# Kernel tuning notes

Measured on AMD Instinct MI355X. Metric: run time of the kernel, lower is better.

Reference implementation:

```python
import jax, jax.numpy as jnp
import numpy as np

B, N = 128, 1024            # batch, sample_count
MIN_S, MAX_S, STEP = 4.0, 104.0, 1.0  # scale range -> S = 101 scales
OUT_H, OUT_W = 200, 200     # output_size


def morlet_kernels():
    # scales = tf.range(min_scale, max_scale+1, step)
    scales = jnp.arange(MIN_S, MAX_S + 1.0, STEP, dtype=jnp.float32)  # (S,)
    t = jnp.arange(N, dtype=jnp.float32) - (N - 1.0) / 2.0            # centered time
    times = t[None, :] / scales[:, None]                               # (S, N)
    return jnp.exp(-0.5 * times ** 2) * jnp.cos(5.0 * times)          # morlet


def setup_inputs() -> dict:
    key = jax.random.key(0)
    x = jax.random.normal(key, (B, N), dtype=jnp.float32)
    kernels = morlet_kernels()  # (S, N), non-trainable param built in build()
    return {"x": x, "kernels": kernels}


def reference(x, kernels):
    # x: (B, N) signals; kernels: (S, N) scaled wavelets.
    # Original per-sample op: conv1d(kernels[S,N,1], filter=reverse(x)[N,1,1], SAME)
    # -> correlation of each wavelet row with the reversed signal (= convolution with x).
    n = x.shape[1]
    pad_l = (n - 1) // 2           # TF 'SAME' padding, stride 1, filter length n
    pad_r = (n - 1) - pad_l
    x_rev = x[:, ::-1]
    # One grouped conv: lhs=(S,1,N) NCW, rhs=(B,1,N) OIW -> out (S,B,N)
    res = jax.lax.conv_general_dilated(
        kernels[:, None, :], x_rev[:, None, :],
        window_strides=(1,), padding=[(pad_l, pad_r)],
        dimension_numbers=("NCW", "OIW", "NCW"))
    res = jnp.transpose(res, (1, 0, 2))  # (B, S, N)
    # global (per-sample) min-max normalization
    mn = jnp.min(res, axis=(1, 2), keepdims=True)
    mx = jnp.max(res, axis=(1, 2), keepdims=True)
    res_norm = (res - mn) / (mx - mn)
    img = res_norm[..., None]  # (B, S, N, 1)
    # tf.image.resize default: bilinear, antialias=False, half-pixel centers
    out = jax.image.resize(img, (img.shape[0], OUT_H, OUT_W, 1),
                           method="bilinear", antialias=False)
    return out
```

## Files before the change

kernel.cpp:

```cpp
#include <hip/hip_runtime.h>
#include <hip/hip_bf16.h>

#define NB 128
#define NS 101
#define NW 1024
#define OH 200
#define OW 200
#define EPS 1034

typedef __bf16 bf16x8 __attribute__((ext_vector_type(8)));
typedef float f32x4 __attribute__((ext_vector_type(4)));


#define STAGE_T(t, lo, hi, base)                                              \
    _Pragma("unroll")                                                         \
    for (int s = (lo); s <= (hi); ++s) {                                      \
        if ((((base) + s - (lo)) & 7) == wv) {                                \
            const int row = 16 * (t) + n;                                     \
            union { ushort us[8]; uint4 v; } pk;                              \
            pk.v = (uint4){0u, 0u, 0u, 0u};                                   \
            if (row < NS) {                                                   \
                const float* kp = K + (size_t)row * NW + 32 * s + 8 * g;      \
                const float4 f0 = *(const float4*)kp;                         \
                const float4 f1 = *(const float4*)(kp + 4);                   \
                __hip_bfloat16 h;                                             \
                h = __float2bfloat16(f0.x); pk.us[0] = reinterpret_cast<const ushort&>(h); \
                h = __float2bfloat16(f0.y); pk.us[1] = reinterpret_cast<const ushort&>(h); \
                h = __float2bfloat16(f0.z); pk.us[2] = reinterpret_cast<const ushort&>(h); \
                h = __float2bfloat16(f0.w); pk.us[3] = reinterpret_cast<const ushort&>(h); \
                h = __float2bfloat16(f1.x); pk.us[4] = reinterpret_cast<const ushort&>(h); \
                h = __float2bfloat16(f1.y); pk.us[5] = reinterpret_cast<const ushort&>(h); \
                h = __float2bfloat16(f1.z); pk.us[6] = reinterpret_cast<const ushort&>(h); \
                h = __float2bfloat16(f1.w); pk.us[7] = reinterpret_cast<const ushort&>(h); \
            }                                                                 \
            *(uint4*)&A_lds[((base) + s - (lo)) * 512 + lane * 8] = pk.v;     \
        }                                                                     \
    }

#define MFMA_T(t, lo, hi, base, ti)                                           \
    if (s >= (lo) && s <= (hi)) {                                             \
        bf16x8 af = *(const bf16x8*)&A_lds[((base) + s - (lo)) * 512 + lane * 8]; \
        _Pragma("unroll")                                                     \
        for (int nt = 0; nt < 8; ++nt)                                        \
            acc[ti][nt] = __builtin_amdgcn_mfma_f32_16x16x32_bf16(            \
                af, ring[(2 * s - nt) & 7], acc[ti][nt], 0, 0, 0);            \
    }

#define EPI_T(t, ti)                                                          \
    {                                                                         \
        _Pragma("unroll")                                                     \
        for (int nt = 0; nt < 8; ++nt) {                                      \
            _Pragma("unroll")                                                 \
            for (int r = 0; r < 4; ++r) {                                     \
                const int row16 = 4 * g + r;                                  \
                float v = acc[ti][nt][r];                                     \
                if (16 * (t) + row16 < NS) { mn = fminf(mn, v); mx = fmaxf(mx, v); } \
                epi[row16 * EPS + wbase + 16 * nt + n] = v;                   \
            }                                                                 \
        }                                                                     \
        __syncthreads();                                                      \
        for (int idx = tid; idx < 16 * OW; idx += 512) {                      \
            const int row16 = idx / OW;                                       \
            const int j = idx % OW;                                           \
            const int srow = 16 * (t) + row16;                                \
            if (srow < NS) {                                                  \
                const float xx = (j + 0.5f) * (1024.0f / 200.0f) - 0.5f;      \
                const float xf = floorf(xx);                                  \
                const float fx = xx - xf;                                     \
                int j0 = (int)xf, j1 = j0 + 1;                                \
                j0 = max(0, min(NW - 1, j0)); j1 = max(0, min(NW - 1, j1));   \
                tmp[((size_t)b * NS + srow) * OW + j] = __float2bfloat16(     \
                    (1.f - fx) * epi[row16 * EPS + j0] + fx * epi[row16 * EPS + j1]); \
            }                                                                 \
        }                                                                     \
        __syncthreads();                                                      \
    }

__global__ __launch_bounds__(512, 1) void conv_mfma(
        const float* __restrict__ x, const float* __restrict__ K,
        __hip_bfloat16* __restrict__ tmp, float* __restrict__ mm) {
    __shared__ __align__(16) char smem[118912];
    ushort* A_lds = (ushort*)smem;
    ushort* xSh = (ushort*)(smem + 86016);
    float* epi = (float*)smem;
    __shared__ float smn[8], smx[8];

    const int tid = threadIdx.x;
    const int bid = blockIdx.x;
    const int cls = bid >> 7;
    const int b = bid & 127;
    const int wv = tid >> 6;
    const int lane = tid & 63;
    const int n = lane & 15;
    const int g = lane >> 4;

    {
        const float* xb = x + (size_t)b * NW;
        for (int idx = tid; idx < 8 * 257; idx += 512) {
            int dlt = idx / 257;
            int i0 = (idx % 257) * 8;
            union { ushort us[8]; uint4 v; } pk;
            #pragma unroll
            for (int j = 0; j < 8; ++j) {
                int ir = i0 + j + dlt;
                float f = (ir >= 512 && ir < 1536) ? xb[1535 - ir] : 0.0f;
                __hip_bfloat16 h = __float2bfloat16(f);
                pk.us[j] = reinterpret_cast<const ushort&>(h);
            }
            *reinterpret_cast<uint4*>(&xSh[dlt * 2056 + i0]) = pk.v;
        }
    }

    if (cls == 0) {
        STAGE_T(0, 12, 19, 0)
        STAGE_T(1,  9, 22, 8)
        STAGE_T(3,  3, 28, 22)
        STAGE_T(4,  0, 31, 48)
    } else {
        STAGE_T(2,  6, 25, 0)
        STAGE_T(5,  0, 31, 20)
        STAGE_T(6,  0, 31, 52)
    }
    __syncthreads();

    const int dlt = (7 - n) & 7;
    const int wbase = wv * 128;
    const ushort* bp = xSh + dlt * 2056 + (1023 - wbase - n + 8 * g - dlt);

    float mn = 3.4e38f, mx = -3.4e38f;

    if (cls == 0) {
        f32x4 acc[4][8];
        #pragma unroll
        for (int ti = 0; ti < 4; ++ti)
            #pragma unroll
            for (int nt = 0; nt < 8; ++nt)
                acc[ti][nt] = (f32x4){0.f, 0.f, 0.f, 0.f};
        bf16x8 ring[8];
        #pragma unroll
        for (int f = -7; f <= 0; ++f)
            ring[f & 7] = *(const bf16x8*)(bp + 16 * f);
        #pragma unroll
        for (int s = 0; s < 32; ++s) {
            if (s > 0) {
                ring[(2 * s - 1) & 7] = *(const bf16x8*)(bp + 16 * (2 * s - 1));
                ring[(2 * s) & 7]     = *(const bf16x8*)(bp + 16 * (2 * s));
            }
            MFMA_T(0, 12, 19, 0, 0)
            MFMA_T(1,  9, 22, 8, 1)
            MFMA_T(3,  3, 28, 22, 2)
            MFMA_T(4,  0, 31, 48, 3)
        }
        __syncthreads();
        EPI_T(0, 0)
        EPI_T(1, 1)
        EPI_T(3, 2)
        EPI_T(4, 3)
    } else {
        f32x4 acc[3][8];
        #pragma unroll
        for (int ti = 0; ti < 3; ++ti)
            #pragma unroll
            for (int nt = 0; nt < 8; ++nt)
                acc[ti][nt] = (f32x4){0.f, 0.f, 0.f, 0.f};
        bf16x8 ring[8];
        #pragma unroll
        for (int f = -7; f <= 0; ++f)
            ring[f & 7] = *(const bf16x8*)(bp + 16 * f);
        #pragma unroll
        for (int s = 0; s < 32; ++s) {
            if (s > 0) {
                ring[(2 * s - 1) & 7] = *(const bf16x8*)(bp + 16 * (2 * s - 1));
                ring[(2 * s) & 7]     = *(const bf16x8*)(bp + 16 * (2 * s));
            }
            MFMA_T(2,  6, 25, 0, 0)
            MFMA_T(5,  0, 31, 20, 1)
            MFMA_T(6,  0, 31, 52, 2)
        }
        __syncthreads();
        EPI_T(2, 0)
        EPI_T(5, 1)
        EPI_T(6, 2)
    }

    #pragma unroll
    for (int off = 32; off > 0; off >>= 1) {
        mn = fminf(mn, __shfl_down(mn, off));
        mx = fmaxf(mx, __shfl_down(mx, off));
    }
    if (lane == 0) { smn[wv] = mn; smx[wv] = mx; }
    __syncthreads();
    if (tid == 0) {
        float bmn = smn[0], bmx = smx[0];
        #pragma unroll
        for (int w = 1; w < 8; ++w) {
            bmn = fminf(bmn, smn[w]);
            bmx = fmaxf(bmx, smx[w]);
        }
        mm[cls * 256 + b] = bmn;
        mm[cls * 256 + 128 + b] = bmx;
    }
}

__global__ __launch_bounds__(256) void resize_v(
        const __hip_bfloat16* __restrict__ tmp, const float* __restrict__ mm,
        float* __restrict__ out) {
    int idx = blockIdx.x * 256 + threadIdx.x;
    if (idx >= NB * OH * OW) return;
    const int j = idx % OW;
    const int i = (idx / OW) % OH;
    const int b = idx / (OW * OH);
    const float mn = fminf(mm[b], mm[256 + b]);
    const float mx = fmaxf(mm[128 + b], mm[384 + b]);
    const float inv = 1.0f / (mx - mn);
    const float y = (i + 0.5f) * (101.0f / 200.0f) - 0.5f;
    const float yf = floorf(y);
    const float fy = y - yf;
    int i0 = (int)yf, i1 = i0 + 1;
    i0 = max(0, min(NS - 1, i0)); i1 = max(0, min(NS - 1, i1));
    const __hip_bfloat16* tp = tmp + (size_t)b * NS * OW;
    float v = (1.f - fy) * __bfloat162float(tp[i0 * OW + j])
            + fy * __bfloat162float(tp[i1 * OW + j]);
    out[idx] = (v - mn) * inv;
}

extern "C" void kernel_launch(void* const* d_in, const int* in_sizes, int n_in,
                              void* d_out, int out_size, void* d_ws, size_t ws_size,
                              hipStream_t stream) {
    const float* x = (const float*)d_in[0];
    const float* K = (const float*)d_in[1];
    float* out = (float*)d_out;

    char* ws = (char*)d_ws;
    float* mm = (float*)ws;
    __hip_bfloat16* tmp = (__hip_bfloat16*)(ws + 4096);

    hipLaunchKernelGGL(conv_mfma, dim3(256), dim3(512), 0, stream, x, K, tmp, mm);
    const int t2 = NB * OH * OW;
    hipLaunchKernelGGL(resize_v, dim3((t2 + 255) / 256), dim3(256), 0, stream, tmp, mm, out);
}
```

Baseline: 99.55 us.

## Split conv work into one block per scale tile with a prep kernel

Adds a prep kernel that converts the wavelet bank and the shifted reversed signals to bf16 in global memory once. The conv kernel now runs one block per (tile, batch), 896 blocks, with a small LDS footprint so up to four blocks fit per CU. Signal copies go through global_load_lds, and wavelet fragments are read directly from global memory with double-buffered prefetch. This trades one extra launch and an extra global round-trip for more parallelism and occupancy than the old 256 heavyweight blocks. Each block writes its own partial min/max, and the resize kernel combines seven of them.

```diff
diff --git a/kernel.cpp b/kernel.cpp
--- a/kernel.cpp
+++ b/kernel.cpp
@@ -11,185 +11,140 @@
 typedef __bf16 bf16x8 __attribute__((ext_vector_type(8)));
 typedef float f32x4 __attribute__((ext_vector_type(4)));
 
-
-#define STAGE_T(t, lo, hi, base)                                              \
-    _Pragma("unroll")                                                         \
-    for (int s = (lo); s <= (hi); ++s) {                                      \
-        if ((((base) + s - (lo)) & 7) == wv) {                                \
-            const int row = 16 * (t) + n;                                     \
-            union { ushort us[8]; uint4 v; } pk;                              \
-            pk.v = (uint4){0u, 0u, 0u, 0u};                                   \
-            if (row < NS) {                                                   \
-                const float* kp = K + (size_t)row * NW + 32 * s + 8 * g;      \
-                const float4 f0 = *(const float4*)kp;                         \
-                const float4 f1 = *(const float4*)(kp + 4);                   \
-                __hip_bfloat16 h;                                             \
-                h = __float2bfloat16(f0.x); pk.us[0] = reinterpret_cast<const ushort&>(h); \
-                h = __float2bfloat16(f0.y); pk.us[1] = reinterpret_cast<const ushort&>(h); \
-                h = __float2bfloat16(f0.z); pk.us[2] = reinterpret_cast<const ushort&>(h); \
-                h = __float2bfloat16(f0.w); pk.us[3] = reinterpret_cast<const ushort&>(h); \
-                h = __float2bfloat16(f1.x); pk.us[4] = reinterpret_cast<const ushort&>(h); \
-                h = __float2bfloat16(f1.y); pk.us[5] = reinterpret_cast<const ushort&>(h); \
-                h = __float2bfloat16(f1.z); pk.us[6] = reinterpret_cast<const ushort&>(h); \
-                h = __float2bfloat16(f1.w); pk.us[7] = reinterpret_cast<const ushort&>(h); \
-            }                                                                 \
-            *(uint4*)&A_lds[((base) + s - (lo)) * 512 + lane * 8] = pk.v;     \
-        }                                                                     \
-    }
-
-#define MFMA_T(t, lo, hi, base, ti)                                           \
-    if (s >= (lo) && s <= (hi)) {                                             \
-        bf16x8 af = *(const bf16x8*)&A_lds[((base) + s - (lo)) * 512 + lane * 8]; \
-        _Pragma("unroll")                                                     \
-        for (int nt = 0; nt < 8; ++nt)                                        \
-            acc[ti][nt] = __builtin_amdgcn_mfma_f32_16x16x32_bf16(            \
-                af, ring[(2 * s - nt) & 7], acc[ti][nt], 0, 0, 0);            \
-    }
-
-#define EPI_T(t, ti)                                                          \
-    {                                                                         \
-        _Pragma("unroll")                                                     \
-        for (int nt = 0; nt < 8; ++nt) {                                      \
-            _Pragma("unroll")                                                 \
-            for (int r = 0; r < 4; ++r) {                                     \
-                const int row16 = 4 * g + r;                                  \
-                float v = acc[ti][nt][r];                                     \
-                if (16 * (t) + row16 < NS) { mn = fminf(mn, v); mx = fmaxf(mx, v); } \
-                epi[row16 * EPS + wbase + 16 * nt + n] = v;                   \
-            }                                                                 \
-        }                                                                     \
-        __syncthreads();                                                      \
-        for (int idx = tid; idx < 16 * OW; idx += 512) {                      \
-            const int row16 = idx / OW;                                       \
-            const int j = idx % OW;                                           \
-            const int srow = 16 * (t) + row16;                                \
-            if (srow < NS) {                                                  \
-                const float xx = (j + 0.5f) * (1024.0f / 200.0f) - 0.5f;      \
-                const float xf = floorf(xx);                                  \
-                const float fx = xx - xf;                                     \
-                int j0 = (int)xf, j1 = j0 + 1;                                \
-                j0 = max(0, min(NW - 1, j0)); j1 = max(0, min(NW - 1, j1));   \
-                tmp[((size_t)b * NS + srow) * OW + j] = __float2bfloat16(     \
-                    (1.f - fx) * epi[row16 * EPS + j0] + fx * epi[row16 * EPS + j1]); \
-            }                                                                 \
-        }                                                                     \
-        __syncthreads();                                                      \
-    }
-
-__global__ __launch_bounds__(512, 1) void conv_mfma(
+__device__ __forceinline__ void gload_lds16(const void* gsrc, void* ldst) {
+    __builtin_amdgcn_global_load_lds(
+        (const __attribute__((address_space(1))) void*)gsrc,
+        (__attribute__((address_space(3))) void*)ldst, 16, 0, 0);
+}
+
+__global__ __launch_bounds__(256) void prep_kernel(
         const float* __restrict__ x, const float* __restrict__ K,
-        __hip_bfloat16* __restrict__ tmp, float* __restrict__ mm) {
-    __shared__ __align__(16) char smem[118912];
-    ushort* A_lds = (ushort*)smem;
-    ushort* xSh = (ushort*)(smem + 86016);
-    float* epi = (float*)smem;
-    __shared__ float smn[8], smx[8];
-
+        ushort* __restrict__ Kbf, ushort* __restrict__ xRsh) {
+    const int b = blockIdx.x;
     const int tid = threadIdx.x;
-    const int bid = blockIdx.x;
-    const int cls = bid >> 7;
-    const int b = bid & 127;
-    const int wv = tid >> 6;
-    const int lane = tid & 63;
-    const int n = lane & 15;
-    const int g = lane >> 4;
+    const float* xb = x + (size_t)b * NW;
+    ushort* dst = xRsh + (size_t)b * 16448;
+    for (int idx = tid; idx < 2056; idx += 256) {
+        const int d = idx / 257;
+        const int i0 = (idx % 257) * 8;
+        union { ushort us[8]; uint4 v; } pk;
+        #pragma unroll
+        for (int j = 0; j < 8; ++j) {
+            const int q = i0 + j + d;
+            float f = (q >= 512 && q < 1536) ? xb[1535 - q] : 0.0f;
+            __hip_bfloat16 h = __float2bfloat16(f);
+            pk.us[j] = reinterpret_cast<const ushort&>(h);
+        }
+        *(uint4*)(dst + d * 2056 + i0) = pk.v;
+    }
+    if (b < 112) {
+        const int c = tid * 4;
+        float4 v = make_float4(0.f, 0.f, 0.f, 0.f);
+        if (b < NS) v = *(const float4*)(K + (size_t)b * NW + c);
+        ushort4 o; __hip_bfloat16 h;
+        h = __float2bfloat16(v.x); o.x = reinterpret_cast<const ushort&>(h);
+        h = __float2bfloat16(v.y); o.y = reinterpret_cast<const ushort&>(h);
+        h = __float2bfloat16(v.z); o.z = reinterpret_cast<const ushort&>(h);
+        h = __float2bfloat16(v.w); o.w = reinterpret_cast<const ushort&>(h);
+        *(ushort4*)(Kbf + (size_t)b * NW + c) = o;
+    }
+}
+
+template<int LO, int HI>
+__device__ __forceinline__ void conv_body(
+        const int t, const int b,
+        const ushort* __restrict__ Kbf, const ushort* __restrict__ xRsh,
+        __hip_bfloat16* __restrict__ tmp, float* __restrict__ mm,
+        ushort* xSh, float* epi, float* smn, float* smx) {
+    const int tid = threadIdx.x;
+    const int wv = tid >> 6, lane = tid & 63, n = lane & 15, g = lane >> 4;
 
     {
-        const float* xb = x + (size_t)b * NW;
-        for (int idx = tid; idx < 8 * 257; idx += 512) {
-            int dlt = idx / 257;
-            int i0 = (idx % 257) * 8;
-            union { ushort us[8]; uint4 v; } pk;
-            #pragma unroll
-            for (int j = 0; j < 8; ++j) {
-                int ir = i0 + j + dlt;
-                float f = (ir >= 512 && ir < 1536) ? xb[1535 - ir] : 0.0f;
-                __hip_bfloat16 h = __float2bfloat16(f);
-                pk.us[j] = reinterpret_cast<const ushort&>(h);
-            }
-            *reinterpret_cast<uint4*>(&xSh[dlt * 2056 + i0]) = pk.v;
-        }
-    }
-
-    if (cls == 0) {
-        STAGE_T(0, 12, 19, 0)
-        STAGE_T(1,  9, 22, 8)
-        STAGE_T(3,  3, 28, 22)
-        STAGE_T(4,  0, 31, 48)
-    } else {
-        STAGE_T(2,  6, 25, 0)
-        STAGE_T(5,  0, 31, 20)
-        STAGE_T(6,  0, 31, 52)
+        const ushort* src = xRsh + (size_t)b * 16448;
+        for (int idx = tid; idx < 2056; idx += 512)
+            gload_lds16(src + (size_t)idx * 8, xSh + idx * 8);
     }
     __syncthreads();
 
     const int dlt = (7 - n) & 7;
     const int wbase = wv * 128;
     const ushort* bp = xSh + dlt * 2056 + (1023 - wbase - n + 8 * g - dlt);
+    const ushort* ap = Kbf + (size_t)(16 * t + n) * NW + 8 * g;
+
+    f32x4 acc[8];
+    #pragma unroll
+    for (int nt = 0; nt < 8; ++nt) acc[nt] = (f32x4){0.f, 0.f, 0.f, 0.f};
+
+    bf16x8 ring[8];
+    #pragma unroll
+    for (int f = 2 * LO - 7; f <= 2 * LO; ++f)
+        ring[f & 7] = *(const bf16x8*)(bp + 16 * f);
+
+    bf16x8 aA = *(const bf16x8*)(ap + 32 * LO);
+    bf16x8 aB = *(const bf16x8*)(ap + 32 * (LO + 1));
+
+    #pragma unroll
+    for (int sp = 0; sp < (HI - LO + 1) / 2; ++sp) {
+        const int s0 = LO + 2 * sp;
+        const int s1 = s0 + 1;
+        if (s0 > LO) {
+            ring[(2 * s0 - 1) & 7] = *(const bf16x8*)(bp + 16 * (2 * s0 - 1));
+            ring[(2 * s0) & 7]     = *(const bf16x8*)(bp + 16 * (2 * s0));
+        }
+        #pragma unroll
+        for (int nt = 0; nt < 8; ++nt)
+            acc[nt] = __builtin_amdgcn_mfma_f32_16x16x32_bf16(
+                aA, ring[(2 * s0 - nt) & 7], acc[nt], 0, 0, 0);
+        if (s0 + 2 <= HI) aA = *(const bf16x8*)(ap + 32 * (s0 + 2));
+        ring[(2 * s1 - 1) & 7] = *(const bf16x8*)(bp + 16 * (2 * s1 - 1));
+        ring[(2 * s1) & 7]     = *(const bf16x8*)(bp + 16 * (2 * s1));
+        #pragma unroll
+        for (int nt = 0; nt < 8; ++nt)
+            acc[nt] = __builtin_amdgcn_mfma_f32_16x16x32_bf16(
+                aB, ring[(2 * s1 - nt) & 7], acc[nt], 0, 0, 0);
+        if (s1 + 2 <= HI) aB = *(const bf16x8*)(ap + 32 * (s1 + 2));
+    }
 
     float mn = 3.4e38f, mx = -3.4e38f;
-
-    if (cls == 0) {
-        f32x4 acc[4][8];
-        #pragma unroll
-        for (int ti = 0; ti < 4; ++ti)
-            #pragma unroll
-            for (int nt = 0; nt < 8; ++nt)
-                acc[ti][nt] = (f32x4){0.f, 0.f, 0.f, 0.f};
-        bf16x8 ring[8];
-        #pragma unroll
-        for (int f = -7; f <= 0; ++f)
-            ring[f & 7] = *(const bf16x8*)(bp + 16 * f);
-        #pragma unroll
-        for (int s = 0; s < 32; ++s) {
-            if (s > 0) {
-                ring[(2 * s - 1) & 7] = *(const bf16x8*)(bp + 16 * (2 * s - 1));
-                ring[(2 * s) & 7]     = *(const bf16x8*)(bp + 16 * (2 * s));
+    #pragma unroll
+    for (int nt = 0; nt < 8; ++nt)
+        #pragma unroll
+        for (int r = 0; r < 4; ++r)
+            if (16 * t + 4 * g + r < NS) {
+                const float v = acc[nt][r];
+                mn = fminf(mn, v); mx = fmaxf(mx, v);
             }
-            MFMA_T(0, 12, 19, 0, 0)
-            MFMA_T(1,  9, 22, 8, 1)
-            MFMA_T(3,  3, 28, 22, 2)
-            MFMA_T(4,  0, 31, 48, 3)
-        }
-        __syncthreads();
-        EPI_T(0, 0)
-        EPI_T(1, 1)
-        EPI_T(3, 2)
-        EPI_T(4, 3)
-    } else {
-        f32x4 acc[3][8];
-        #pragma unroll
-        for (int ti = 0; ti < 3; ++ti)
-            #pragma unroll
-            for (int nt = 0; nt < 8; ++nt)
-                acc[ti][nt] = (f32x4){0.f, 0.f, 0.f, 0.f};
-        bf16x8 ring[8];
-        #pragma unroll
-        for (int f = -7; f <= 0; ++f)
-            ring[f & 7] = *(const bf16x8*)(bp + 16 * f);
-        #pragma unroll
-        for (int s = 0; s < 32; ++s) {
-            if (s > 0) {
-                ring[(2 * s - 1) & 7] = *(const bf16x8*)(bp + 16 * (2 * s - 1));
-                ring[(2 * s) & 7]     = *(const bf16x8*)(bp + 16 * (2 * s));
-            }
-            MFMA_T(2,  6, 25, 0, 0)
-            MFMA_T(5,  0, 31, 20, 1)
-            MFMA_T(6,  0, 31, 52, 2)
-        }
-        __syncthreads();
-        EPI_T(2, 0)
-        EPI_T(5, 1)
-        EPI_T(6, 2)
-    }
-
     #pragma unroll
     for (int off = 32; off > 0; off >>= 1) {
         mn = fminf(mn, __shfl_down(mn, off));
         mx = fmaxf(mx, __shfl_down(mx, off));
     }
     if (lane == 0) { smn[wv] = mn; smx[wv] = mx; }
+
     __syncthreads();
+
+    #pragma unroll
+    for (int nt = 0; nt < 8; ++nt)
+        #pragma unroll
+        for (int r = 0; r < 4; ++r)
+            epi[(4 * g + r) * EPS + wbase + 16 * nt + n] = acc[nt][r];
+    __syncthreads();
+
+    for (int idx = tid; idx < 16 * OW; idx += 512) {
+        const int row16 = idx / OW;
+        const int j = idx % OW;
+        const int srow = 16 * t + row16;
+        if (srow < NS) {
+            const float xx = (j + 0.5f) * (1024.0f / 200.0f) - 0.5f;
+            const float xf = floorf(xx);
+            const float fx = xx - xf;
+            int j0 = (int)xf, j1 = j0 + 1;
+            j0 = max(0, min(NW - 1, j0)); j1 = max(0, min(NW - 1, j1));
+            tmp[((size_t)b * NS + srow) * OW + j] = __float2bfloat16(
+                (1.f - fx) * epi[row16 * EPS + j0] + fx * epi[row16 * EPS + j1]);
+        }
+    }
+
     if (tid == 0) {
         float bmn = smn[0], bmx = smx[0];
         #pragma unroll
@@ -197,8 +152,29 @@
             bmn = fminf(bmn, smn[w]);
             bmx = fmaxf(bmx, smx[w]);
         }
-        mm[cls * 256 + b] = bmn;
-        mm[cls * 256 + 128 + b] = bmx;
+        mm[t * 256 + b] = bmn;
+        mm[t * 256 + 128 + b] = bmx;
+    }
+}
+
+__global__ __launch_bounds__(512, 4) void conv_mfma(
+        const ushort* __restrict__ Kbf, const ushort* __restrict__ xRsh,
+        __hip_bfloat16* __restrict__ tmp, float* __restrict__ mm) {
+    __shared__ __align__(16) char smem[16 * EPS * 4];
+    __shared__ float smn[8], smx[8];
+    ushort* xSh = (ushort*)smem;
+    float* epi = (float*)smem;
+
+    const int cls = blockIdx.x >> 7;
+    const int b = blockIdx.x & 127;
+    const int t = (cls < 3) ? cls + 4 : 6 - cls;
+
+    switch (t) {
+        case 0: conv_body<12, 19>(t, b, Kbf, xRsh, tmp, mm, xSh, epi, smn, smx); break;
+        case 1: conv_body< 9, 22>(t, b, Kbf, xRsh, tmp, mm, xSh, epi, smn, smx); break;
+        case 2: conv_body< 6, 25>(t, b, Kbf, xRsh, tmp, mm, xSh, epi, smn, smx); break;
+        case 3: conv_body< 3, 28>(t, b, Kbf, xRsh, tmp, mm, xSh, epi, smn, smx); break;
+        default: conv_body<0, 31>(t, b, Kbf, xRsh, tmp, mm, xSh, epi, smn, smx); break;
     }
 }
 
@@ -210,8 +186,12 @@
     const int j = idx % OW;
     const int i = (idx / OW) % OH;
     const int b = idx / (OW * OH);
-    const float mn = fminf(mm[b], mm[256 + b]);
-    const float mx = fmaxf(mm[128 + b], mm[384 + b]);
+    float mn = mm[b], mx = mm[128 + b];
+    #pragma unroll
+    for (int t = 1; t < 7; ++t) {
+        mn = fminf(mn, mm[t * 256 + b]);
+        mx = fmaxf(mx, mm[t * 256 + 128 + b]);
+    }
     const float inv = 1.0f / (mx - mn);
     const float y = (i + 0.5f) * (101.0f / 200.0f) - 0.5f;
     const float yf = floorf(y);
@@ -219,8 +199,8 @@
     int i0 = (int)yf, i1 = i0 + 1;
     i0 = max(0, min(NS - 1, i0)); i1 = max(0, min(NS - 1, i1));
     const __hip_bfloat16* tp = tmp + (size_t)b * NS * OW;
-    float v = (1.f - fy) * __bfloat162float(tp[i0 * OW + j])
-            + fy * __bfloat162float(tp[i1 * OW + j]);
+    const float v = (1.f - fy) * __bfloat162float(tp[i0 * OW + j])
+                  + fy * __bfloat162float(tp[i1 * OW + j]);
     out[idx] = (v - mn) * inv;
 }
 
@@ -233,9 +213,12 @@
 
     char* ws = (char*)d_ws;
     float* mm = (float*)ws;
-    __hip_bfloat16* tmp = (__hip_bfloat16*)(ws + 4096);
-
-    hipLaunchKernelGGL(conv_mfma, dim3(256), dim3(512), 0, stream, x, K, tmp, mm);
+    ushort* Kbf = (ushort*)(ws + 8192);
+    ushort* xRsh = (ushort*)(ws + 8192 + 229376);
+    __hip_bfloat16* tmp = (__hip_bfloat16*)(ws + 4448256);
+
+    hipLaunchKernelGGL(prep_kernel, dim3(128), dim3(256), 0, stream, x, K, Kbf, xRsh);
+    hipLaunchKernelGGL(conv_mfma, dim3(896), dim3(512), 0, stream, Kbf, xRsh, tmp, mm);
     const int t2 = NB * OH * OW;
     hipLaunchKernelGGL(resize_v, dim3((t2 + 255) / 256), dim3(256), 0, stream, tmp, mm, out);
 }
```

Measured after the change: 112.4 us. 12.9% more time.
